# Optimization experiments

Measured on AMD Instinct MI355X. Metric: run time of the kernel, lower is better.

Reference implementation:

```python
import jax, jax.numpy as jnp
import numpy as np

C = 36   # num_classes
H = 256  # hidden_dim


def setup_inputs() -> dict:
    key = jax.random.key(0)
    ks = jax.random.split(key, 12)
    B, L, Dl, Dg = 32, 196, 1024, 1024
    s = lambda d: 1.0 / np.sqrt(d)
    return {
        "local_features": jax.random.normal(ks[0], (B, L, Dl), jnp.float32),
        "global_average_pool": jax.random.normal(ks[1], (B, Dg), jnp.float32),
        "Wl": jax.random.normal(ks[2], (Dl, C * H), jnp.float32) * s(Dl),
        "bl": jax.random.normal(ks[3], (C * H,), jnp.float32) * s(Dl),
        "Wg": jax.random.normal(ks[4], (Dg, C * H), jnp.float32) * s(Dg),
        "bg": jax.random.normal(ks[5], (C * H,), jnp.float32) * s(Dg),
        "Wh": jax.random.normal(ks[6], (H, H), jnp.float32) * s(H),
        "bh": jax.random.normal(ks[7], (H,), jnp.float32) * s(H),
        "Wr": jax.random.normal(ks[8], (H, 4), jnp.float32) * s(H),
        "br": jax.random.normal(ks[9], (4,), jnp.float32) * s(H),
        "Wc": jax.random.normal(ks[10], (H, 1), jnp.float32) * s(H),
        "bc": jax.random.normal(ks[11], (1,), jnp.float32) * s(H),
    }


def reference(local_features, global_average_pool, Wl, bl, Wg, bg, Wh, bh, Wr, br, Wc, bc):
    B, L, _ = local_features.shape
    # global projection -> [B, C, H]
    xg = (global_average_pool @ Wg + bg).reshape(B, C, H)
    # local projection -> [B, L, C, H] -> [B, C, L, H]
    xl = (local_features @ Wl + bl).reshape(B, L, C, H).transpose(0, 2, 1, 3)
    # per-class attention scores over locations: [B, C, L]
    dot = jnp.einsum('bch,bclh->bcl', xg, xl)
    attn = jax.nn.softmax(dot, axis=-1)
    # attention-weighted sum over locations: [B, C, H]
    ws = jnp.einsum('bcl,bclh->bch', attn, xl)
    hid = jax.nn.relu(ws @ Wh + bh)
    bbox_coords = (hid @ Wr + br).reshape(B, C * 4)   # [B, 4C]
    bbox_presence = (hid @ Wc + bc)[..., 0]           # [B, C]
    return bbox_coords, bbox_presence
```

## Files before the change

### kernel.cpp

```cpp
#include <hip/hip_runtime.h>
#include <stdint.h>

#define NCLS 36
#define HDIM 256
#define BSZ  32
#define LLOC 196
#define DIN  1024
#define NCH  9216
#define NCH4 2304
#define XG_N 294912
#define SC_N 225792
#define V_N  1179648

__device__ __forceinline__ void fma4(float4& a, float s, const float4& b) {
  a.x += s * b.x; a.y += s * b.y; a.z += s * b.z; a.w += s * b.w;
}
__device__ __forceinline__ float dot4(const float4& a, const float4& b) {
  return a.x * b.x + a.y * b.y + a.z * b.z + a.w * b.w;
}

__global__ __launch_bounds__(256) void kA_xg(
    const float* __restrict__ Wg, const float* __restrict__ gap,
    float* __restrict__ XGP) {
  __shared__ __align__(16) float4 gs[512];
  const int tid = threadIdx.x;
  const int nt = blockIdx.x, ks = blockIdx.y;
  const int n0 = nt * 256, k0 = ks * 64;
  const float4* gap4 = (const float4*)gap;
  for (int i = tid; i < 512; i += 256)
    gs[i] = gap4[(size_t)(i >> 4) * 256 + ks * 16 + (i & 15)];
  __syncthreads();
  const int ng = tid & 31, bq = tid >> 5;
  const int b0 = bq * 4;
  float4 acc0[4] = {}; float4 acc1[4] = {};
  const float* wp = Wg + (size_t)k0 * NCH + n0 + ng * 4;
  for (int k4 = 0; k4 < 16; ++k4) {
    float4 w0[4], w1[4];
    #pragma unroll
    for (int kk = 0; kk < 4; ++kk) {
      const float* p = wp + (size_t)(k4 * 4 + kk) * NCH;
      w0[kk] = *(const float4*)p;
      w1[kk] = *(const float4*)(p + 128);
    }
    #pragma unroll
    for (int bb = 0; bb < 4; ++bb) {
      float4 g = gs[(b0 + bb) * 16 + k4];
      fma4(acc0[bb], g.x, w0[0]); fma4(acc0[bb], g.y, w0[1]);
      fma4(acc0[bb], g.z, w0[2]); fma4(acc0[bb], g.w, w0[3]);
      fma4(acc1[bb], g.x, w1[0]); fma4(acc1[bb], g.y, w1[1]);
      fma4(acc1[bb], g.z, w1[2]); fma4(acc1[bb], g.w, w1[3]);
    }
  }
  #pragma unroll
  for (int bb = 0; bb < 4; ++bb) {
    size_t o = (size_t)ks * XG_N + (size_t)(b0 + bb) * NCH + n0 + ng * 4;
    *(float4*)&XGP[o]       = acc0[bb];
    *(float4*)&XGP[o + 128] = acc1[bb];
  }
}

__global__ __launch_bounds__(256) void kB_red(
    const float* __restrict__ XGP, float* __restrict__ XG) {
  const int i = blockIdx.x * 256 + threadIdx.x;
  const float4* p4 = (const float4*)XGP;
  float4 s = p4[i];
  #pragma unroll
  for (int p = 1; p < 16; ++p) {
    float4 t = p4[(size_t)p * (XG_N / 4) + i];
    s.x += t.x; s.y += t.y; s.z += t.z; s.w += t.w;
  }
  ((float4*)XG)[i] = s;
}

__global__ __launch_bounds__(512) void kC_V(
    const float* __restrict__ Wl, const float* __restrict__ XG,
    const float* __restrict__ bg, float* __restrict__ V) {
  __shared__ __align__(16) float4 xs[2048];
  const int tid = threadIdx.x;
  const int c = blockIdx.x, kt = blockIdx.y;
  const float4* xg4 = (const float4*)XG;
  const float4* bg4 = (const float4*)bg;
  for (int i = tid; i < 2048; i += 512) {
    int b = i >> 6, h4 = i & 63;
    float4 t = xg4[(size_t)b * NCH4 + c * 64 + h4];
    float4 bv = bg4[c * 64 + h4];
    t.x += bv.x; t.y += bv.y; t.z += bv.z; t.w += bv.w;
    xs[i] = t;
  }
  __syncthreads();
  const int lane = tid & 63, w = tid >> 6;
  const int q = lane & 3, r = lane >> 2;
  const int b0 = w * 4;
  const int krow = kt * 128 + r * 8;
  float acc[4][8] = {};
  const float* wl = Wl + (size_t)krow * NCH + c * 256 + q * 4;
  for (int it = 0; it < 16; ++it) {
    float4 wv[8];
    #pragma unroll
    for (int kk = 0; kk < 8; ++kk)
      wv[kk] = *(const float4*)(wl + (size_t)kk * NCH + it * 16);
    #pragma unroll
    for (int bb = 0; bb < 4; ++bb) {
      float4 x = xs[(b0 + bb) * 64 + it * 4 + q];
      #pragma unroll
      for (int kk = 0; kk < 8; ++kk)
        acc[bb][kk] += dot4(wv[kk], x);
    }
  }
  #pragma unroll
  for (int bb = 0; bb < 4; ++bb) {
    #pragma unroll
    for (int kk = 0; kk < 8; ++kk) {
      float s = acc[bb][kk];
      s += __shfl_xor(s, 1); s += __shfl_xor(s, 2);
      acc[bb][kk] = s;
    }
  }
  if (q == 0) {
    #pragma unroll
    for (int bb = 0; bb < 4; ++bb)
      #pragma unroll
      for (int kk = 0; kk < 8; ++kk)
        V[(size_t)((b0 + bb) * NCLS + c) * DIN + krow + kk] = acc[bb][kk];
  }
}

__global__ __launch_bounds__(256) void kD_scores(
    const float* __restrict__ local_f, const float* __restrict__ V,
    float* __restrict__ SCP) {
  __shared__ __align__(16) float4 loc_s[3136];
  __shared__ __align__(16) float4 v_s[576];
  const int tid = threadIdx.x;
  const int b = blockIdx.x, ks = blockIdx.y;
  const float4* lf4 = (const float4*)local_f;
  for (int i = tid; i < 3136; i += 256) {
    int r = i >> 4, g = i & 15;
    loc_s[r * 16 + ((g + r) & 15)] = lf4[(size_t)(b * LLOC + r) * 256 + ks * 16 + g];
  }
  const float4* v4 = (const float4*)V;
  for (int i = tid; i < 576; i += 256) {
    int cc = i >> 4, g = i & 15;
    v_s[i] = v4[(size_t)(b * NCLS + cc) * 256 + ks * 16 + g];
  }
  __syncthreads();
  const int lg = tid & 63, cg = tid >> 6;
  float acc[4][9] = {};
  for (int k4 = 0; k4 < 16; ++k4) {
    float4 vv[9];
    #pragma unroll
    for (int ci = 0; ci < 9; ++ci) vv[ci] = v_s[(cg * 9 + ci) * 16 + k4];
    #pragma unroll
    for (int i = 0; i < 4; ++i) {
      int l = lg + 64 * i;
      if (l < LLOC) {
        float4 a = loc_s[l * 16 + ((k4 + l) & 15)];
        #pragma unroll
        for (int ci = 0; ci < 9; ++ci) acc[i][ci] += dot4(a, vv[ci]);
      }
    }
  }
  #pragma unroll
  for (int i = 0; i < 4; ++i) {
    int l = lg + 64 * i;
    if (l < LLOC) {
      #pragma unroll
      for (int ci = 0; ci < 9; ++ci)
        SCP[(size_t)ks * SC_N + (size_t)(b * NCLS + cg * 9 + ci) * LLOC + l] = acc[i][ci];
    }
  }
}

__global__ __launch_bounds__(64) void kE_softmax(
    const float* __restrict__ SCP, float* __restrict__ attn2) {
  const int b = blockIdx.x, c = blockIdx.y, t = threadIdx.x;
  const size_t base = (size_t)(b * NCLS + c) * LLOC;
  float sc[4];
  int nl = 0;
  float m = -1e30f;
  for (int l = t; l < LLOC; l += 64) {
    float s = 0.f;
    #pragma unroll
    for (int p = 0; p < 16; ++p) s += SCP[(size_t)p * SC_N + base + l];
    sc[nl++] = s; m = fmaxf(m, s);
  }
  #pragma unroll
  for (int off = 32; off >= 1; off >>= 1) m = fmaxf(m, __shfl_xor(m, off));
  float sum = 0.f;
  for (int i = 0; i < nl; ++i) { sc[i] = __expf(sc[i] - m); sum += sc[i]; }
  #pragma unroll
  for (int off = 32; off >= 1; off >>= 1) sum += __shfl_xor(sum, off);
  float inv = 1.0f / sum;
  nl = 0;
  for (int l = t; l < LLOC; l += 64) attn2[base + l] = sc[nl++] * inv;
}

__global__ __launch_bounds__(256) void kF_U(
    const float* __restrict__ local_f, const float* __restrict__ ATT,
    float* __restrict__ U) {
  __shared__ __align__(16) float4 att_s[1764];
  __shared__ __align__(16) float4 red[4608];
  const int tid = threadIdx.x;
  const int b = blockIdx.x, ks = blockIdx.y;
  const int k0 = ks * 128;
  const float4* at4 = (const float4*)ATT;
  for (int i = tid; i < 1764; i += 256) {
    int cc = i / 49, l4 = i - cc * 49;
    att_s[i] = at4[(size_t)(b * NCLS + cc) * 49 + l4];
  }
  __syncthreads();
  const int kg = tid & 15, cg = (tid >> 4) & 3, lh = tid >> 6;
  float4 acc[9][2] = {};
  const float* lbase = local_f + (size_t)b * LLOC * DIN + k0 + kg * 8;
  for (int l4 = lh; l4 < 49; l4 += 4) {
    float4 lv[4][2];
    #pragma unroll
    for (int ll = 0; ll < 4; ++ll) {
      const float* p = lbase + (size_t)(l4 * 4 + ll) * DIN;
      lv[ll][0] = *(const float4*)p;
      lv[ll][1] = *(const float4*)(p + 4);
    }
    #pragma unroll
    for (int ci = 0; ci < 9; ++ci) {
      float4 av = att_s[(cg * 9 + ci) * 49 + l4];
      fma4(acc[ci][0], av.x, lv[0][0]); fma4(acc[ci][1], av.x, lv[0][1]);
      fma4(acc[ci][0], av.y, lv[1][0]); fma4(acc[ci][1], av.y, lv[1][1]);
      fma4(acc[ci][0], av.z, lv[2][0]); fma4(acc[ci][1], av.z, lv[2][1]);
      fma4(acc[ci][0], av.w, lv[3][0]); fma4(acc[ci][1], av.w, lv[3][1]);
    }
  }
  #pragma unroll
  for (int ci = 0; ci < 9; ++ci) {
    int c = cg * 9 + ci;
    red[lh * 1152 + c * 32 + kg * 2 + 0] = acc[ci][0];
    red[lh * 1152 + c * 32 + kg * 2 + 1] = acc[ci][1];
  }
  __syncthreads();
  float4* u4 = (float4*)U;
  for (int i = tid; i < 1152; i += 256) {
    float4 s = red[i];
    #pragma unroll
    for (int p = 1; p < 4; ++p) {
      float4 t = red[p * 1152 + i];
      s.x += t.x; s.y += t.y; s.z += t.z; s.w += t.w;
    }
    u4[(size_t)(b * NCLS + (i >> 5)) * 256 + ks * 32 + (i & 31)] = s;
  }
}

__global__ __launch_bounds__(256) void kG_ws(
    const float* __restrict__ Wl, const float* __restrict__ U,
    float* __restrict__ WSP) {
  __shared__ __align__(16) float4 us[512];
  const int tid = threadIdx.x;
  const int c = blockIdx.x, ks = blockIdx.y;
  const int k0 = ks * 64;
  const float4* u4 = (const float4*)U;
  for (int i = tid; i < 512; i += 256)
    us[i] = u4[(size_t)((i >> 4) * NCLS + c) * 256 + ks * 16 + (i & 15)];
  __syncthreads();
  const int ng = tid & 31, bq = tid >> 5;
  const int b0 = bq * 4;
  float4 acc0[4] = {}; float4 acc1[4] = {};
  const float* wp = Wl + (size_t)k0 * NCH + c * 256 + ng * 4;
  for (int k4 = 0; k4 < 16; ++k4) {
    float4 w0[4], w1[4];
    #pragma unroll
    for (int kk = 0; kk < 4; ++kk) {
      const float* p = wp + (size_t)(k4 * 4 + kk) * NCH;
      w0[kk] = *(const float4*)p;
      w1[kk] = *(const float4*)(p + 128);
    }
    #pragma unroll
    for (int bb = 0; bb < 4; ++bb) {
      float4 g = us[(b0 + bb) * 16 + k4];
      fma4(acc0[bb], g.x, w0[0]); fma4(acc0[bb], g.y, w0[1]);
      fma4(acc0[bb], g.z, w0[2]); fma4(acc0[bb], g.w, w0[3]);
      fma4(acc1[bb], g.x, w1[0]); fma4(acc1[bb], g.y, w1[1]);
      fma4(acc1[bb], g.z, w1[2]); fma4(acc1[bb], g.w, w1[3]);
    }
  }
  #pragma unroll
  for (int bb = 0; bb < 4; ++bb) {
    size_t o = (size_t)ks * XG_N + (size_t)(b0 + bb) * NCH + c * 256 + ng * 4;
    *(float4*)&WSP[o]       = acc0[bb];
    *(float4*)&WSP[o + 128] = acc1[bb];
  }
}

__global__ __launch_bounds__(256) void kH_heads(
    const float* __restrict__ Wh, const float* __restrict__ bh,
    const float* __restrict__ Wr, const float* __restrict__ br,
    const float* __restrict__ Wc, const float* __restrict__ bc,
    const float* __restrict__ bl,
    const float* __restrict__ WSP, float* __restrict__ out) {
  __shared__ float ws_s[3][HDIM];
  __shared__ float hid_s[3][HDIM];
  const int b = blockIdx.x, c0 = blockIdx.y * 3;
  const int j = threadIdx.x;
  #pragma unroll
  for (int ci = 0; ci < 3; ++ci) {
    size_t base = (size_t)b * NCH + (c0 + ci) * HDIM + j;
    float s = bl[(c0 + ci) * HDIM + j];
    #pragma unroll
    for (int p = 0; p < 16; ++p) s += WSP[(size_t)p * XG_N + base];
    ws_s[ci][j] = s;
  }
  __syncthreads();
  float acc[3] = {0, 0, 0};
  for (int h = 0; h < HDIM; ++h) {
    float whj = Wh[(size_t)h * HDIM + j];
    acc[0] += ws_s[0][h] * whj;
    acc[1] += ws_s[1][h] * whj;
    acc[2] += ws_s[2][h] * whj;
  }
  float bj = bh[j];
  #pragma unroll
  for (int ci = 0; ci < 3; ++ci) hid_s[ci][j] = fmaxf(acc[ci] + bj, 0.0f);
  __syncthreads();
  const int r = j >> 6, j0 = j & 63;
  for (int ci = 0; ci < 3; ++ci) {
    const int c = c0 + ci;
    float s = 0.f;
    #pragma unroll
    for (int m = 0; m < 4; ++m)
      s += hid_s[ci][j0 + 64 * m] * Wr[(j0 + 64 * m) * 4 + r];
    #pragma unroll
    for (int off = 32; off >= 1; off >>= 1) s += __shfl_xor(s, off);
    if (j0 == 0) out[(size_t)b * (NCLS * 4) + c * 4 + r] = s + br[r];
    if (r == 0) {
      float p = 0.f;
      #pragma unroll
      for (int m = 0; m < 4; ++m)
        p += hid_s[ci][j0 + 64 * m] * Wc[j0 + 64 * m];
      #pragma unroll
      for (int off = 32; off >= 1; off >>= 1) p += __shfl_xor(p, off);
      if (j0 == 0) out[BSZ * NCLS * 4 + b * NCLS + c] = p + bc[0];
    }
  }
}

extern "C" void kernel_launch(void* const* d_in, const int* in_sizes, int n_in,
                              void* d_out, int out_size, void* d_ws, size_t ws_size,
                              hipStream_t stream) {
  const float* local = (const float*)d_in[0];
  const float* gap   = (const float*)d_in[1];
  const float* Wl    = (const float*)d_in[2];
  const float* bl    = (const float*)d_in[3];
  const float* Wg    = (const float*)d_in[4];
  const float* bg    = (const float*)d_in[5];
  const float* Wh    = (const float*)d_in[6];
  const float* bh    = (const float*)d_in[7];
  const float* Wr    = (const float*)d_in[8];
  const float* br    = (const float*)d_in[9];
  const float* Wc    = (const float*)d_in[10];
  const float* bc    = (const float*)d_in[11];
  float* out         = (float*)d_out;

  float* XGP = (float*)d_ws;
  float* XG  = XGP + (size_t)16 * XG_N;
  float* V   = XG + XG_N;
  float* SCP = V + V_N;
  float* ATT = SCP + (size_t)16 * SC_N;
  float* U   = ATT + SC_N;
  float* WSP = U + V_N;

  kA_xg     <<<dim3(36, 16), dim3(256), 0, stream>>>(Wg, gap, XGP);
  kB_red    <<<dim3(288),    dim3(256), 0, stream>>>(XGP, XG);
  kC_V      <<<dim3(36, 8),  dim3(512), 0, stream>>>(Wl, XG, bg, V);
  kD_scores <<<dim3(32, 16), dim3(256), 0, stream>>>(local, V, SCP);
  kE_softmax<<<dim3(32, 36), dim3(64),  0, stream>>>(SCP, ATT);
  kF_U      <<<dim3(32, 8),  dim3(256), 0, stream>>>(local, ATT, U);
  kG_ws     <<<dim3(36, 16), dim3(256), 0, stream>>>(Wl, U, WSP);
  kH_heads  <<<dim3(32, 12), dim3(256), 0, stream>>>(Wh, bh, Wr, br, Wc, bc, bl, WSP, out);
}
```

Measured before the change: 271.2 us.

## Retile weight GEMV kernels, fold bias into reduction, vectorize softmax

The Wg and Wl weight-streaming kernels (kA, kG) now use narrower N tiles of 128 and deeper K splits of 128, which halves the number of partial-sum slices from 16 to 8. kB and kH reduce fewer partials, and the bg bias add moves from kC into kB. kC_V is retiled to 128-thread blocks, each thread handling 2 K rows for 16 batches, giving more blocks and less register pressure. The softmax reads and writes float4 for its partial-sum reduction, at the cost of idle lanes for threads past 49.

```diff
diff --git a/kernel.cpp b/kernel.cpp
--- a/kernel.cpp
+++ b/kernel.cpp
@@ -10,6 +10,7 @@
 #define NCH4 2304
 #define XG_N 294912
 #define SC_N 225792
+#define SC_N4 56448
 #define V_N  1179648
 
 __device__ __forceinline__ void fma4(float4& a, float s, const float4& b) {
@@ -22,106 +23,95 @@
 __global__ __launch_bounds__(256) void kA_xg(
     const float* __restrict__ Wg, const float* __restrict__ gap,
     float* __restrict__ XGP) {
-  __shared__ __align__(16) float4 gs[512];
+  __shared__ __align__(16) float4 gs[1024];
   const int tid = threadIdx.x;
   const int nt = blockIdx.x, ks = blockIdx.y;
-  const int n0 = nt * 256, k0 = ks * 64;
+  const int n0 = nt * 128, k0 = ks * 128;
   const float4* gap4 = (const float4*)gap;
-  for (int i = tid; i < 512; i += 256)
-    gs[i] = gap4[(size_t)(i >> 4) * 256 + ks * 16 + (i & 15)];
-  __syncthreads();
-  const int ng = tid & 31, bq = tid >> 5;
-  const int b0 = bq * 4;
-  float4 acc0[4] = {}; float4 acc1[4] = {};
+  for (int i = tid; i < 1024; i += 256)
+    gs[i] = gap4[(size_t)(i >> 5) * 256 + ks * 32 + (i & 31)];
+  __syncthreads();
+  const int ng = tid & 31, b0 = (tid >> 5) * 4;
+  float4 acc[4] = {};
   const float* wp = Wg + (size_t)k0 * NCH + n0 + ng * 4;
-  for (int k4 = 0; k4 < 16; ++k4) {
-    float4 w0[4], w1[4];
-    #pragma unroll
-    for (int kk = 0; kk < 4; ++kk) {
-      const float* p = wp + (size_t)(k4 * 4 + kk) * NCH;
-      w0[kk] = *(const float4*)p;
-      w1[kk] = *(const float4*)(p + 128);
-    }
+  #pragma unroll 4
+  for (int k4 = 0; k4 < 32; ++k4) {
+    float4 w[4];
+    #pragma unroll
+    for (int kk = 0; kk < 4; ++kk)
+      w[kk] = *(const float4*)(wp + (size_t)(k4 * 4 + kk) * NCH);
     #pragma unroll
     for (int bb = 0; bb < 4; ++bb) {
-      float4 g = gs[(b0 + bb) * 16 + k4];
-      fma4(acc0[bb], g.x, w0[0]); fma4(acc0[bb], g.y, w0[1]);
-      fma4(acc0[bb], g.z, w0[2]); fma4(acc0[bb], g.w, w0[3]);
-      fma4(acc1[bb], g.x, w1[0]); fma4(acc1[bb], g.y, w1[1]);
-      fma4(acc1[bb], g.z, w1[2]); fma4(acc1[bb], g.w, w1[3]);
-    }
-  }
-  #pragma unroll
-  for (int bb = 0; bb < 4; ++bb) {
-    size_t o = (size_t)ks * XG_N + (size_t)(b0 + bb) * NCH + n0 + ng * 4;
-    *(float4*)&XGP[o]       = acc0[bb];
-    *(float4*)&XGP[o + 128] = acc1[bb];
-  }
+      float4 g = gs[(b0 + bb) * 32 + k4];
+      fma4(acc[bb], g.x, w[0]); fma4(acc[bb], g.y, w[1]);
+      fma4(acc[bb], g.z, w[2]); fma4(acc[bb], g.w, w[3]);
+    }
+  }
+  #pragma unroll
+  for (int bb = 0; bb < 4; ++bb)
+    *(float4*)&XGP[(size_t)ks * XG_N + (size_t)(b0 + bb) * NCH + n0 + ng * 4] = acc[bb];
 }
 
 __global__ __launch_bounds__(256) void kB_red(
-    const float* __restrict__ XGP, float* __restrict__ XG) {
-  const int i = blockIdx.x * 256 + threadIdx.x;
+    const float* __restrict__ XGP, const float* __restrict__ bg,
+    float* __restrict__ XG) {
+  const int b = blockIdx.x / 9;
+  const int j = (blockIdx.x % 9) * 256 + threadIdx.x;
+  const size_t off = (size_t)b * NCH4 + j;
   const float4* p4 = (const float4*)XGP;
-  float4 s = p4[i];
-  #pragma unroll
-  for (int p = 1; p < 16; ++p) {
-    float4 t = p4[(size_t)p * (XG_N / 4) + i];
+  float4 s = ((const float4*)bg)[j];
+  #pragma unroll
+  for (int p = 0; p < 8; ++p) {
+    float4 t = p4[(size_t)p * (XG_N / 4) + off];
     s.x += t.x; s.y += t.y; s.z += t.z; s.w += t.w;
   }
-  ((float4*)XG)[i] = s;
-}
-
-__global__ __launch_bounds__(512) void kC_V(
+  ((float4*)XG)[off] = s;
+}
+
+__global__ __launch_bounds__(128) void kC_V(
     const float* __restrict__ Wl, const float* __restrict__ XG,
-    const float* __restrict__ bg, float* __restrict__ V) {
+    float* __restrict__ V) {
   __shared__ __align__(16) float4 xs[2048];
   const int tid = threadIdx.x;
   const int c = blockIdx.x, kt = blockIdx.y;
+  const int k0 = kt * 32;
   const float4* xg4 = (const float4*)XG;
-  const float4* bg4 = (const float4*)bg;
-  for (int i = tid; i < 2048; i += 512) {
+  for (int i = tid; i < 2048; i += 128) {
     int b = i >> 6, h4 = i & 63;
-    float4 t = xg4[(size_t)b * NCH4 + c * 64 + h4];
-    float4 bv = bg4[c * 64 + h4];
-    t.x += bv.x; t.y += bv.y; t.z += bv.z; t.w += bv.w;
-    xs[i] = t;
-  }
-  __syncthreads();
-  const int lane = tid & 63, w = tid >> 6;
+    xs[i] = xg4[(size_t)b * NCH4 + c * 64 + h4];
+  }
+  __syncthreads();
+  const int lane = tid & 63, wv_ = tid >> 6;
   const int q = lane & 3, r = lane >> 2;
-  const int b0 = w * 4;
-  const int krow = kt * 128 + r * 8;
-  float acc[4][8] = {};
+  const int b0 = wv_ * 16;
+  const int krow = k0 + r * 2;
+  float acc0[16] = {}; float acc1[16] = {};
   const float* wl = Wl + (size_t)krow * NCH + c * 256 + q * 4;
+  #pragma unroll 4
   for (int it = 0; it < 16; ++it) {
-    float4 wv[8];
-    #pragma unroll
-    for (int kk = 0; kk < 8; ++kk)
-      wv[kk] = *(const float4*)(wl + (size_t)kk * NCH + it * 16);
-    #pragma unroll
-    for (int bb = 0; bb < 4; ++bb) {
+    float4 w0 = *(const float4*)(wl + it * 16);
+    float4 w1 = *(const float4*)(wl + NCH + it * 16);
+    #pragma unroll
+    for (int bb = 0; bb < 16; ++bb) {
       float4 x = xs[(b0 + bb) * 64 + it * 4 + q];
-      #pragma unroll
-      for (int kk = 0; kk < 8; ++kk)
-        acc[bb][kk] += dot4(wv[kk], x);
-    }
-  }
-  #pragma unroll
-  for (int bb = 0; bb < 4; ++bb) {
-    #pragma unroll
-    for (int kk = 0; kk < 8; ++kk) {
-      float s = acc[bb][kk];
-      s += __shfl_xor(s, 1); s += __shfl_xor(s, 2);
-      acc[bb][kk] = s;
-    }
+      acc0[bb] += dot4(w0, x);
+      acc1[bb] += dot4(w1, x);
+    }
+  }
+  #pragma unroll
+  for (int bb = 0; bb < 16; ++bb) {
+    float s0 = acc0[bb], s1 = acc1[bb];
+    s0 += __shfl_xor(s0, 1); s0 += __shfl_xor(s0, 2);
+    s1 += __shfl_xor(s1, 1); s1 += __shfl_xor(s1, 2);
+    acc0[bb] = s0; acc1[bb] = s1;
   }
   if (q == 0) {
     #pragma unroll
-    for (int bb = 0; bb < 4; ++bb)
-      #pragma unroll
-      for (int kk = 0; kk < 8; ++kk)
-        V[(size_t)((b0 + bb) * NCLS + c) * DIN + krow + kk] = acc[bb][kk];
+    for (int bb = 0; bb < 16; ++bb) {
+      size_t o = (size_t)((b0 + bb) * NCLS + c) * DIN + krow;
+      V[o]     = acc0[bb];
+      V[o + 1] = acc1[bb];
+    }
   }
 }
 
@@ -171,27 +161,37 @@
 }
 
 __global__ __launch_bounds__(64) void kE_softmax(
-    const float* __restrict__ SCP, float* __restrict__ attn2) {
+    const float* __restrict__ SCP, float* __restrict__ ATT) {
   const int b = blockIdx.x, c = blockIdx.y, t = threadIdx.x;
-  const size_t base = (size_t)(b * NCLS + c) * LLOC;
-  float sc[4];
-  int nl = 0;
+  const size_t base4 = (size_t)(b * NCLS + c) * 49;
+  const float4* s4 = (const float4*)SCP;
+  float4 s = {0.f, 0.f, 0.f, 0.f};
   float m = -1e30f;
-  for (int l = t; l < LLOC; l += 64) {
-    float s = 0.f;
-    #pragma unroll
-    for (int p = 0; p < 16; ++p) s += SCP[(size_t)p * SC_N + base + l];
-    sc[nl++] = s; m = fmaxf(m, s);
+  if (t < 49) {
+    s = s4[base4 + t];
+    #pragma unroll
+    for (int p = 1; p < 16; ++p) {
+      float4 x = s4[(size_t)p * SC_N4 + base4 + t];
+      s.x += x.x; s.y += x.y; s.z += x.z; s.w += x.w;
+    }
+    m = fmaxf(fmaxf(s.x, s.y), fmaxf(s.z, s.w));
   }
   #pragma unroll
   for (int off = 32; off >= 1; off >>= 1) m = fmaxf(m, __shfl_xor(m, off));
+  float4 e = {0.f, 0.f, 0.f, 0.f};
   float sum = 0.f;
-  for (int i = 0; i < nl; ++i) { sc[i] = __expf(sc[i] - m); sum += sc[i]; }
+  if (t < 49) {
+    e.x = __expf(s.x - m); e.y = __expf(s.y - m);
+    e.z = __expf(s.z - m); e.w = __expf(s.w - m);
+    sum = e.x + e.y + e.z + e.w;
+  }
   #pragma unroll
   for (int off = 32; off >= 1; off >>= 1) sum += __shfl_xor(sum, off);
   float inv = 1.0f / sum;
-  nl = 0;
-  for (int l = t; l < LLOC; l += 64) attn2[base + l] = sc[nl++] * inv;
+  if (t < 49) {
+    e.x *= inv; e.y *= inv; e.z *= inv; e.w *= inv;
+    ((float4*)ATT)[base4 + t] = e;
+  }
 }
 
 __global__ __launch_bounds__(256) void kF_U(
@@ -250,41 +250,34 @@
 __global__ __launch_bounds__(256) void kG_ws(
     const float* __restrict__ Wl, const float* __restrict__ U,
     float* __restrict__ WSP) {
-  __shared__ __align__(16) float4 us[512];
-  const int tid = threadIdx.x;
-  const int c = blockIdx.x, ks = blockIdx.y;
-  const int k0 = ks * 64;
+  __shared__ __align__(16) float4 us[1024];
+  const int tid = threadIdx.x;
+  const int nt = blockIdx.x, ks = blockIdx.y;
+  const int c = nt >> 1, h0 = (nt & 1) * 128, k0 = ks * 128;
   const float4* u4 = (const float4*)U;
-  for (int i = tid; i < 512; i += 256)
-    us[i] = u4[(size_t)((i >> 4) * NCLS + c) * 256 + ks * 16 + (i & 15)];
-  __syncthreads();
-  const int ng = tid & 31, bq = tid >> 5;
-  const int b0 = bq * 4;
-  float4 acc0[4] = {}; float4 acc1[4] = {};
-  const float* wp = Wl + (size_t)k0 * NCH + c * 256 + ng * 4;
-  for (int k4 = 0; k4 < 16; ++k4) {
-    float4 w0[4], w1[4];
-    #pragma unroll
-    for (int kk = 0; kk < 4; ++kk) {
-      const float* p = wp + (size_t)(k4 * 4 + kk) * NCH;
-      w0[kk] = *(const float4*)p;
-      w1[kk] = *(const float4*)(p + 128);
-    }
+  for (int i = tid; i < 1024; i += 256)
+    us[i] = u4[(size_t)((i >> 5) * NCLS + c) * 256 + ks * 32 + (i & 31)];
+  __syncthreads();
+  const int ng = tid & 31, b0 = (tid >> 5) * 4;
+  float4 acc[4] = {};
+  const float* wp = Wl + (size_t)k0 * NCH + c * HDIM + h0 + ng * 4;
+  #pragma unroll 4
+  for (int k4 = 0; k4 < 32; ++k4) {
+    float4 w[4];
+    #pragma unroll
+    for (int kk = 0; kk < 4; ++kk)
+      w[kk] = *(const float4*)(wp + (size_t)(k4 * 4 + kk) * NCH);
     #pragma unroll
     for (int bb = 0; bb < 4; ++bb) {
-      float4 g = us[(b0 + bb) * 16 + k4];
-      fma4(acc0[bb], g.x, w0[0]); fma4(acc0[bb], g.y, w0[1]);
-      fma4(acc0[bb], g.z, w0[2]); fma4(acc0[bb], g.w, w0[3]);
-      fma4(acc1[bb], g.x, w1[0]); fma4(acc1[bb], g.y, w1[1]);
-      fma4(acc1[bb], g.z, w1[2]); fma4(acc1[bb], g.w, w1[3]);
-    }
-  }
-  #pragma unroll
-  for (int bb = 0; bb < 4; ++bb) {
-    size_t o = (size_t)ks * XG_N + (size_t)(b0 + bb) * NCH + c * 256 + ng * 4;
-    *(float4*)&WSP[o]       = acc0[bb];
-    *(float4*)&WSP[o + 128] = acc1[bb];
-  }
+      float4 g = us[(b0 + bb) * 32 + k4];
+      fma4(acc[bb], g.x, w[0]); fma4(acc[bb], g.y, w[1]);
+      fma4(acc[bb], g.z, w[2]); fma4(acc[bb], g.w, w[3]);
+    }
+  }
+  #pragma unroll
+  for (int bb = 0; bb < 4; ++bb)
+    *(float4*)&WSP[(size_t)ks * XG_N + (size_t)(b0 + bb) * NCH + c * HDIM + h0 + ng * 4]
+        = acc[bb];
 }
 
 __global__ __launch_bounds__(256) void kH_heads(
@@ -302,7 +295,7 @@
     size_t base = (size_t)b * NCH + (c0 + ci) * HDIM + j;
     float s = bl[(c0 + ci) * HDIM + j];
     #pragma unroll
-    for (int p = 0; p < 16; ++p) s += WSP[(size_t)p * XG_N + base];
+    for (int p = 0; p < 8; ++p) s += WSP[(size_t)p * XG_N + base];
     ws_s[ci][j] = s;
   }
   __syncthreads();
@@ -357,19 +350,19 @@
   float* out         = (float*)d_out;
 
   float* XGP = (float*)d_ws;
-  float* XG  = XGP + (size_t)16 * XG_N;
+  float* XG  = XGP + (size_t)8 * XG_N;
   float* V   = XG + XG_N;
   float* SCP = V + V_N;
   float* ATT = SCP + (size_t)16 * SC_N;
   float* U   = ATT + SC_N;
   float* WSP = U + V_N;
 
-  kA_xg     <<<dim3(36, 16), dim3(256), 0, stream>>>(Wg, gap, XGP);
-  kB_red    <<<dim3(288),    dim3(256), 0, stream>>>(XGP, XG);
-  kC_V      <<<dim3(36, 8),  dim3(512), 0, stream>>>(Wl, XG, bg, V);
+  kA_xg     <<<dim3(72, 8),  dim3(256), 0, stream>>>(Wg, gap, XGP);
+  kB_red    <<<dim3(288),    dim3(256), 0, stream>>>(XGP, bg, XG);
+  kC_V      <<<dim3(36, 32), dim3(128), 0, stream>>>(Wl, XG, V);
   kD_scores <<<dim3(32, 16), dim3(256), 0, stream>>>(local, V, SCP);
   kE_softmax<<<dim3(32, 36), dim3(64),  0, stream>>>(SCP, ATT);
   kF_U      <<<dim3(32, 8),  dim3(256), 0, stream>>>(local, ATT, U);
-  kG_ws     <<<dim3(36, 16), dim3(256), 0, stream>>>(Wl, U, WSP);
+  kG_ws     <<<dim3(72, 8),  dim3(256), 0, stream>>>(Wl, U, WSP);
   kH_heads  <<<dim3(32, 12), dim3(256), 0, stream>>>(Wh, bh, Wr, br, Wc, bc, bl, WSP, out);
 }
```

Result: slower. 288.3 us (+6.3%).
